# Optimization experiments

Measured on AMD Instinct MI355X. Metric: run time of the kernel, lower is better.

## Reference

```python
import jax, jax.numpy as jnp
import numpy as np

PATCH = [2, 4, 8, 16]   # square window sizes, one per head group
LAYERS = 2
C = 128                 # channel = d_input = hidden
DK = C // len(PATCH)    # 32 channels per head group


def leaky(z):
    return jax.nn.leaky_relu(z, negative_slope=0.2)


def conv2d(x, w, b, dil=1, pad=1):
    # x: (N,C,H,W), w: (O,I,3,3)
    y = jax.lax.conv_general_dilated(
        x, w, window_strides=(1, 1), padding=((pad, pad), (pad, pad)),
        rhs_dilation=(dil, dil), dimension_numbers=('NCHW', 'OIHW', 'NCHW'))
    return y + b[None, :, None, None]


def window_attn(q, k, v, bsz, ph, pw):
    # q/k/v: (b*t, dk, h, w) -> attention over t*oh*ow patch tokens of dim dk*ph*pw
    bt, dk, h, w = q.shape
    t = bt // bsz
    oh, ow = h // ph, w // pw

    def to_tok(z):
        z = z.reshape(bsz, t, dk, oh, ph, ow, pw)
        z = z.transpose(0, 1, 3, 5, 2, 4, 6)  # (b, t, oh, ow, dk, ph, pw)
        return z.reshape(bsz, t * oh * ow, dk * ph * pw)

    qt, kt, vt = to_tok(q), to_tok(k), to_tok(v)
    scale = 1.0 / jnp.sqrt(jnp.asarray(qt.shape[-1], qt.dtype))
    scores = jnp.einsum('bld,bmd->blm', qt, kt) * scale
    p = jax.nn.softmax(scores, axis=-1)
    y = jnp.einsum('blm,bmd->bld', p, vt)
    y = y.reshape(bsz, t, oh, ow, dk, ph, pw).transpose(0, 1, 4, 2, 5, 3, 6)
    return y.reshape(bt, dk, h, w)


def transformer_block(x, Wq, bq, Wk, bk, Wv, bv, Wo, bo, Wf1, bf1, Wf2, bf2, bsz):
    # 1x1 conv embeddings as channel matmuls
    q = jnp.einsum('bihw,oi->bohw', x, Wq) + bq[None, :, None, None]
    k = jnp.einsum('bihw,oi->bohw', x, Wk) + bk[None, :, None, None]
    v = jnp.einsum('bihw,oi->bohw', x, Wv) + bv[None, :, None, None]
    outs = []
    for g, p in enumerate(PATCH):
        sl = slice(g * DK, (g + 1) * DK)
        outs.append(window_attn(q[:, sl], k[:, sl], v[:, sl], bsz, p, p))
    att = jnp.concatenate(outs, axis=1)
    x = x + leaky(conv2d(att, Wo, bo, dil=1, pad=1))
    f = leaky(conv2d(x, Wf1, bf1, dil=2, pad=2))
    f = leaky(conv2d(f, Wf2, bf2, dil=1, pad=1))
    return x + f


def setup_inputs() -> dict:
    key = jax.random.key(0)
    ks = jax.random.split(key, 14)
    g = 0.02  # init gain matching init_weights normal(0, 0.02)
    x = jax.random.normal(ks[0], (8, C, 64, 64), dtype=jnp.float32)
    mk = lambda k, shape: (g * jax.random.normal(k, shape)).astype(jnp.float32)
    return {
        'x': x,
        'Wq': mk(ks[1], (LAYERS, C, C)), 'bq': jnp.zeros((LAYERS, C), jnp.float32),
        'Wk': mk(ks[2], (LAYERS, C, C)), 'bk': jnp.zeros((LAYERS, C), jnp.float32),
        'Wv': mk(ks[3], (LAYERS, C, C)), 'bv': jnp.zeros((LAYERS, C), jnp.float32),
        'Wo': mk(ks[4], (LAYERS, C, C, 3, 3)), 'bo': jnp.zeros((LAYERS, C), jnp.float32),
        'Wf1': mk(ks[5], (LAYERS, C, C, 3, 3)), 'bf1': jnp.zeros((LAYERS, C), jnp.float32),
        'Wf2': mk(ks[6], (LAYERS, C, C, 3, 3)), 'bf2': jnp.zeros((LAYERS, C), jnp.float32),
        'bsz': 2,
    }


def reference(x, Wq, bq, Wk, bk, Wv, bv, Wo, bo, Wf1, bf1, Wf2, bf2, bsz):
    for i in range(LAYERS):
        x = transformer_block(x, Wq[i], bq[i], Wk[i], bk[i], Wv[i], bv[i],
                              Wo[i], bo[i], Wf1[i], bf1[i], Wf2[i], bf2[i], bsz)
    return x
```

## Files before the change

kernel.cpp:

```cpp
#include <hip/hip_runtime.h>

__device__ __forceinline__ unsigned short f2bf(float f) {
  union { float f; unsigned int i; } c; c.f = f;
  unsigned int i = c.i;
  i += 0x7fffu + ((i >> 16) & 1u);
  return (unsigned short)(i >> 16);
}

typedef __attribute__((ext_vector_type(8))) short bf16x8;
typedef __attribute__((ext_vector_type(4))) float f32x4;


__global__ __launch_bounds__(256) void x2hwc(const float* __restrict__ X,
                                             unsigned short* __restrict__ Xh) {
  int pixg = blockIdx.x * 256 + threadIdx.x;
  int c0 = blockIdx.y * 8;
  int bt = pixg >> 12, pix = pixg & 4095;
  const float* src = X + ((size_t)bt << 19) + (size_t)c0 * 4096 + pix;
  unsigned int pk[4];
#pragma unroll
  for (int j = 0; j < 4; j++) {
    unsigned short u0 = f2bf(src[(2 * j) * 4096]);
    unsigned short u1 = f2bf(src[(2 * j + 1) * 4096]);
    pk[j] = (unsigned int)u0 | ((unsigned int)u1 << 16);
  }
  *(uint4*)(Xh + (size_t)pixg * 128 + c0) = make_uint4(pk[0], pk[1], pk[2], pk[3]);
}

__global__ __launch_bounds__(256) void wprep3(
    const float* __restrict__ s0, const float* __restrict__ s1,
    const float* __restrict__ s2, unsigned short* __restrict__ d0,
    unsigned short* __restrict__ d1, unsigned short* __restrict__ d2) {
  int idx = blockIdx.x * 256 + threadIdx.x;
  const float* s = blockIdx.y == 0 ? s0 : (blockIdx.y == 1 ? s1 : s2);
  unsigned short* d = blockIdx.y == 0 ? d0 : (blockIdx.y == 1 ? d1 : d2);
  int j = idx & 7;
  int lane = (idx >> 3) & 63;
  int kg = lane >> 4, ml = lane & 15;
  int f = idx >> 9;
  int mf = f & 3, wm = (f >> 2) & 1, cs = (f >> 3) & 3, tap = f >> 5;
  int o = wm * 64 + mf * 16 + ml;
  int i = cs * 32 + kg * 8 + j;
  d[idx] = f2bf(s[(size_t)(o * 128 + i) * 9 + tap]);
}

__global__ __launch_bounds__(256) void wprep1(
    const float* __restrict__ s0, const float* __restrict__ s1,
    const float* __restrict__ s2, unsigned short* __restrict__ d0,
    unsigned short* __restrict__ d1, unsigned short* __restrict__ d2) {
  int idx = blockIdx.x * 256 + threadIdx.x;
  const float* s = blockIdx.y == 0 ? s0 : (blockIdx.y == 1 ? s1 : s2);
  unsigned short* d = blockIdx.y == 0 ? d0 : (blockIdx.y == 1 ? d1 : d2);
  d[idx] = f2bf(s[idx]);
}

template <int MODE>
__global__ __launch_bounds__(256) void qkv_pack(
    const unsigned short* __restrict__ Xh, const unsigned short* __restrict__ Wb,
    const float* __restrict__ Bi, unsigned short* __restrict__ P,
    unsigned short* __restrict__ VtP, unsigned short* __restrict__ Ff) {
  int tid = threadIdx.x, lane = tid & 63, wid = tid >> 6;
  int wm = wid & 1, wn = wid >> 1;
  int ml = lane & 15, kg = lane >> 4;
  int m_base = blockIdx.y * 64 + wm * 32;
  int n_base = blockIdx.x * 64 + wn * 32;
  f32x4 acc[2][2];
#pragma unroll
  for (int i = 0; i < 2; i++)
#pragma unroll
    for (int j = 0; j < 2; j++) acc[i][j] = {0.f, 0.f, 0.f, 0.f};
#pragma unroll
  for (int kc = 0; kc < 128; kc += 32) {
    bf16x8 af[2], bfr[2];
#pragma unroll
    for (int mf = 0; mf < 2; mf++)
      af[mf] = *(const bf16x8*)(Wb + (size_t)(m_base + mf * 16 + ml) * 128 + kc + kg * 8);
#pragma unroll
    for (int nf = 0; nf < 2; nf++)
      bfr[nf] = *(const bf16x8*)(Xh + (size_t)(n_base + nf * 16 + ml) * 128 + kc + kg * 8);
#pragma unroll
    for (int mf = 0; mf < 2; mf++)
#pragma unroll
      for (int nf = 0; nf < 2; nf++)
        acc[mf][nf] = __builtin_amdgcn_mfma_f32_16x16x32_bf16(af[mf], bfr[nf], acc[mf][nf], 0, 0, 0);
  }
#pragma unroll
  for (int mf = 0; mf < 2; mf++)
#pragma unroll
    for (int nf = 0; nf < 2; nf++)
#pragma unroll
      for (int r = 0; r < 4; r++) {
        int c = m_base + mf * 16 + kg * 4 + r;
        int pixg = n_base + nf * 16 + ml;
        float val = acc[mf][nf][r] + Bi[c];
        int bt = pixg >> 12, pix = pixg & 4095;
        int h = pix >> 6, w = pix & 63;
        int g = c >> 5, sh = g + 1, msk = (1 << sh) - 1, ohn = 64 >> sh;
        int b = bt >> 2, t_i = bt & 3;
        int l = (t_i * ohn + (h >> sh)) * ohn + (w >> sh);
        int Dg = 32 << (2 * sh);
        int d = ((c & 31) << (2 * sh)) + ((h & msk) << sh) + (w & msk);
        if (MODE == 0) val *= rsqrtf((float)Dg);
        unsigned short bv = f2bf(val);
        size_t bofs = (size_t)b << 19;
        if (g == 0) {
          if (MODE == 0) {
            int qt = l >> 4, mlq = l & 15, cc = d >> 5, kgq = (d >> 3) & 3, j = d & 7;
            Ff[bofs + ((size_t)(qt * 4 + cc) << 9) + (kgq * 16 + mlq) * 8 + j] = bv;
          } else if (MODE == 1) {
            int ck = l >> 6, mfk = (l >> 4) & 3, mlk = l & 15;
            int cc = d >> 5, kgk = (d >> 3) & 3, j = d & 7;
            Ff[bofs + ((size_t)(ck * 16 + cc * 4 + mfk) << 9) + (kgk * 16 + mlk) * 8 + j] = bv;
          } else {
            int ck = l >> 6, part = (l >> 5) & 1, kgv = (l >> 3) & 3, j = l & 7;
            int nf = d >> 4, mlv = d & 15;
            Ff[bofs + ((size_t)(ck * 16 + nf * 2 + part) << 9) + (kgv * 16 + mlv) * 8 + j] = bv;
          }
        } else {
          size_t base = ((size_t)g << 20) + bofs;
          if (MODE != 2) {
            P[base + (size_t)l * Dg + d] = bv;
          } else {
            int Lg = 16384 >> (2 * sh);
            VtP[base + (size_t)d * Lg + l] = bv;
          }
        }
      }
}

__global__ __launch_bounds__(256) void gemm_tn(
    const unsigned short* __restrict__ A, const unsigned short* __restrict__ B,
    float* __restrict__ C, int K, int lda, int ldb, int ldc,
    long long sA, long long sB, long long sC) {
  int tid = threadIdx.x, lane = tid & 63, wid = tid >> 6;
  int wm = wid & 1, wn = wid >> 1;
  int ml = lane & 15, kg = lane >> 4;
  A += (size_t)blockIdx.z * sA;
  B += (size_t)blockIdx.z * sB;
  C += (size_t)blockIdx.z * sC;
  int m_base = blockIdx.y * 64 + wm * 32;
  int n_base = blockIdx.x * 64 + wn * 32;
  f32x4 acc[2][2];
#pragma unroll
  for (int i = 0; i < 2; i++)
#pragma unroll
    for (int j = 0; j < 2; j++) acc[i][j] = {0.f, 0.f, 0.f, 0.f};
  for (int kc = 0; kc < K; kc += 32) {
    bf16x8 af[2], bfr[2];
#pragma unroll
    for (int mf = 0; mf < 2; mf++)
      af[mf] = *(const bf16x8*)(A + (size_t)(m_base + mf * 16 + ml) * lda + kc + kg * 8);
#pragma unroll
    for (int nf = 0; nf < 2; nf++)
      bfr[nf] = *(const bf16x8*)(B + (size_t)(n_base + nf * 16 + ml) * ldb + kc + kg * 8);
#pragma unroll
    for (int mf = 0; mf < 2; mf++)
#pragma unroll
      for (int nf = 0; nf < 2; nf++)
        acc[mf][nf] = __builtin_amdgcn_mfma_f32_16x16x32_bf16(af[mf], bfr[nf], acc[mf][nf], 0, 0, 0);
  }
#pragma unroll
  for (int mf = 0; mf < 2; mf++)
#pragma unroll
    for (int nf = 0; nf < 2; nf++)
#pragma unroll
      for (int r = 0; r < 4; r++) {
        int m = m_base + mf * 16 + kg * 4 + r;
        int n = n_base + nf * 16 + ml;
        C[(size_t)m * ldc + n] = acc[mf][nf][r];
      }
}

__global__ __launch_bounds__(256) void gemm_tn_sk(
    const unsigned short* __restrict__ A, const unsigned short* __restrict__ B,
    float* __restrict__ Cp, int lda, int ldb, int L,
    long long sA, long long sB) {
  constexpr int KC = 128;
  int tid = threadIdx.x, lane = tid & 63, wid = tid >> 6;
  int wm = wid & 1, wn = wid >> 1;
  int ml = lane & 15, kg = lane >> 4;
  int bz = blockIdx.z, b = bz & 1, split = bz >> 1;
  A += (size_t)b * sA + split * KC;
  B += (size_t)b * sB + split * KC;
  float* Ct = Cp + (size_t)bz * L * L;
  int m_base = blockIdx.y * 64 + wm * 32;
  int n_base = blockIdx.x * 64 + wn * 32;
  f32x4 acc[2][2];
#pragma unroll
  for (int i = 0; i < 2; i++)
#pragma unroll
    for (int j = 0; j < 2; j++) acc[i][j] = {0.f, 0.f, 0.f, 0.f};
#pragma unroll
  for (int kc = 0; kc < KC; kc += 32) {
    bf16x8 af[2], bfr[2];
#pragma unroll
    for (int mf = 0; mf < 2; mf++)
      af[mf] = *(const bf16x8*)(A + (size_t)(m_base + mf * 16 + ml) * lda + kc + kg * 8);
#pragma unroll
    for (int nf = 0; nf < 2; nf++)
      bfr[nf] = *(const bf16x8*)(B + (size_t)(n_base + nf * 16 + ml) * ldb + kc + kg * 8);
#pragma unroll
    for (int mf = 0; mf < 2; mf++)
#pragma unroll
      for (int nf = 0; nf < 2; nf++)
        acc[mf][nf] = __builtin_amdgcn_mfma_f32_16x16x32_bf16(af[mf], bfr[nf], acc[mf][nf], 0, 0, 0);
  }
#pragma unroll
  for (int mf = 0; mf < 2; mf++)
#pragma unroll
    for (int nf = 0; nf < 2; nf++)
#pragma unroll
      for (int r = 0; r < 4; r++) {
        int m = m_base + mf * 16 + kg * 4 + r;
        int n = n_base + nf * 16 + ml;
        Ct[(size_t)m * L + n] = acc[mf][nf][r];
      }
}

__global__ __launch_bounds__(256) void gemm_tn_sk2(
    const unsigned short* __restrict__ A, const unsigned short* __restrict__ B,
    float* __restrict__ Cp, int KC, int lda, int ldb, int ldc,
    long long sA, long long sB) {
  int tid = threadIdx.x, lane = tid & 63, wid = tid >> 6;
  int wm = wid & 1, wn = wid >> 1;
  int ml = lane & 15, kg = lane >> 4;
  int bz = blockIdx.z, b = bz & 1, split = bz >> 1;
  A += (size_t)b * sA + (size_t)split * KC;
  B += (size_t)b * sB + (size_t)split * KC;
  size_t MN = (size_t)gridDim.y * 64 * ldc;
  float* Ct = Cp + (size_t)bz * MN;
  int m_base = blockIdx.y * 64 + wm * 32;
  int n_base = blockIdx.x * 64 + wn * 32;
  f32x4 acc[2][2];
#pragma unroll
  for (int i = 0; i < 2; i++)
#pragma unroll
    for (int j = 0; j < 2; j++) acc[i][j] = {0.f, 0.f, 0.f, 0.f};
  for (int kc = 0; kc < KC; kc += 32) {
    bf16x8 af[2], bfr[2];
#pragma unroll
    for (int mf = 0; mf < 2; mf++)
      af[mf] = *(const bf16x8*)(A + (size_t)(m_base + mf * 16 + ml) * lda + kc + kg * 8);
#pragma unroll
    for (int nf = 0; nf < 2; nf++)
      bfr[nf] = *(const bf16x8*)(B + (size_t)(n_base + nf * 16 + ml) * ldb + kc + kg * 8);
#pragma unroll
    for (int mf = 0; mf < 2; mf++)
#pragma unroll
      for (int nf = 0; nf < 2; nf++)
        acc[mf][nf] = __builtin_amdgcn_mfma_f32_16x16x32_bf16(af[mf], bfr[nf], acc[mf][nf], 0, 0, 0);
  }
#pragma unroll
  for (int mf = 0; mf < 2; mf++)
#pragma unroll
    for (int nf = 0; nf < 2; nf++)
#pragma unroll
      for (int r = 0; r < 4; r++) {
        int m = m_base + mf * 16 + kg * 4 + r;
        int n = n_base + nf * 16 + ml;
        Ct[(size_t)m * ldc + n] = acc[mf][nf][r];
      }
}

__global__ __launch_bounds__(256) void sum2(const float* __restrict__ Cp,
                                            float* __restrict__ Out,
                                            int MNq, long long sOut) {
  int idx = blockIdx.x * 256 + threadIdx.x;
  int b = idx / MNq, r = idx - b * MNq;
  const float4* c4 = (const float4*)Cp;
  float4 v0 = c4[(size_t)b * MNq + r];
  float4 v1 = c4[(size_t)(2 + b) * MNq + r];
  float4 o = make_float4(v0.x + v1.x, v0.y + v1.y, v0.z + v1.z, v0.w + v1.w);
  ((float4*)(Out + (size_t)b * sOut))[r] = o;
}

__global__ __launch_bounds__(256) void softmax_sum_bf16(
    const float* __restrict__ Sp, unsigned short* __restrict__ P, int L, int nsplit) {
  __shared__ float red[256];
  int tid = threadIdx.x;
  int b = blockIdx.x / L, m = blockIdx.x - b * L;
  const float* row = Sp + ((size_t)b * L + m) * L;
  long long pstride = 2LL * L * L;
  float val = 0.f;
  if (tid < L) {
    for (int s = 0; s < nsplit; s++) val += row[(size_t)s * pstride + tid];
  }
  red[tid] = (tid < L) ? val : -1e30f;
  __syncthreads();
  for (int s = 128; s > 0; s >>= 1) {
    if (tid < s) red[tid] = fmaxf(red[tid], red[tid + s]);
    __syncthreads();
  }
  float mx = red[0]; __syncthreads();
  float e = (tid < L) ? __expf(val - mx) : 0.f;
  red[tid] = e; __syncthreads();
  for (int s = 128; s > 0; s >>= 1) {
    if (tid < s) red[tid] += red[tid + s];
    __syncthreads();
  }
  float inv = 1.f / red[0];
  if (tid < L) P[((size_t)b * L + m) * L + tid] = f2bf(e * inv);
}

__global__ __launch_bounds__(256) void softmax_bf16(float* __restrict__ S,
                                                    unsigned short* __restrict__ P, int L) {
  __shared__ float red[256];
  int tid = threadIdx.x;
  float* p = S + (size_t)blockIdx.x * L;
  unsigned short* o = P + (size_t)blockIdx.x * L;
  float mx = -1e30f;
  for (int e = tid; e < L; e += 256) mx = fmaxf(mx, p[e]);
  red[tid] = mx; __syncthreads();
  for (int s = 128; s > 0; s >>= 1) {
    if (tid < s) red[tid] = fmaxf(red[tid], red[tid + s]);
    __syncthreads();
  }
  mx = red[0]; __syncthreads();
  float sm = 0.f;
  for (int e = tid; e < L; e += 256) {
    float v = __expf(p[e] - mx);
    p[e] = v; sm += v;
  }
  red[tid] = sm; __syncthreads();
  for (int s = 128; s > 0; s >>= 1) {
    if (tid < s) red[tid] += red[tid + s];
    __syncthreads();
  }
  float inv = 1.f / red[0];
  for (int e = tid; e < L; e += 256) o[e] = f2bf(p[e] * inv);
}

__global__ __launch_bounds__(256, 3) void flash_mfma(
    const unsigned short* __restrict__ Qf, const unsigned short* __restrict__ Kf,
    const unsigned short* __restrict__ Vf, float* __restrict__ Opart,
    float* __restrict__ MLp) {
  __shared__ float Ot[4][16][128];
  __shared__ unsigned short Pl[4][16][72];
  __shared__ float Ml[4][16], Ll[4][16];
  int tid = threadIdx.x, lane = tid & 63, wv = tid >> 6;
  int ml = lane & 15, kg = lane >> 4;
  int b = blockIdx.x >> 8, qt = blockIdx.x & 255;
  int half = blockIdx.y;
  size_t bofs = (size_t)b << 19;
  int q0 = qt * 16;

  bf16x8 qf[4];
#pragma unroll
  for (int cc = 0; cc < 4; cc++)
    qf[cc] = *(const bf16x8*)(Qf + bofs + ((size_t)(qt * 4 + cc) << 9) + lane * 8);

  float m_i = -1e30f, l_i = 0.f;
  f32x4 of[8];
#pragma unroll
  for (int nf = 0; nf < 8; nf++) of[nf] = {0.f, 0.f, 0.f, 0.f};

  int ck0 = half * 32 + wv * 8;
  for (int ck = ck0; ck < ck0 + 8; ck++) {
    const unsigned short* Kc = Kf + bofs + ((size_t)ck << 13);
    const unsigned short* Vc = Vf + bofs + ((size_t)ck << 13);
    f32x4 st[4];
#pragma unroll
    for (int mf = 0; mf < 4; mf++) st[mf] = {0.f, 0.f, 0.f, 0.f};
    __builtin_amdgcn_s_setprio(1);
#pragma unroll
    for (int cc = 0; cc < 4; cc++)
#pragma unroll
      for (int mf = 0; mf < 4; mf++) {
        bf16x8 kf = *(const bf16x8*)(Kc + ((cc * 4 + mf) << 9) + lane * 8);
        st[mf] = __builtin_amdgcn_mfma_f32_16x16x32_bf16(kf, qf[cc], st[mf], 0, 0, 0);
      }
    __builtin_amdgcn_s_setprio(0);
    bf16x8 vf[16];
#pragma unroll
    for (int nv = 0; nv < 16; nv++)
      vf[nv] = *(const bf16x8*)(Vc + (nv << 9) + lane * 8);
    float cmax = -1e30f;
#pragma unroll
    for (int mf = 0; mf < 4; mf++)
#pragma unroll
      for (int r = 0; r < 4; r++) cmax = fmaxf(cmax, st[mf][r]);
    cmax = fmaxf(cmax, __shfl_xor(cmax, 16));
    cmax = fmaxf(cmax, __shfl_xor(cmax, 32));
    int skip = __all(cmax <= m_i);
    float mnew = skip ? m_i : fmaxf(m_i, cmax);
    float p[4][4];
    float psum = 0.f;
#pragma unroll
    for (int mf = 0; mf < 4; mf++)
#pragma unroll
      for (int r = 0; r < 4; r++) {
        float pv = __expf(st[mf][r] - mnew);
        p[mf][r] = pv; psum += pv;
      }
    psum += __shfl_xor(psum, 16);
    psum += __shfl_xor(psum, 32);
    if (skip) {
      l_i += psum;
    } else {
      float alpha = __expf(m_i - mnew);
      l_i = l_i * alpha + psum;
      m_i = mnew;
      float a0 = __shfl(alpha, kg * 4 + 0), a1 = __shfl(alpha, kg * 4 + 1);
      float a2 = __shfl(alpha, kg * 4 + 2), a3 = __shfl(alpha, kg * 4 + 3);
#pragma unroll
      for (int nf = 0; nf < 8; nf++) {
        of[nf][0] *= a0; of[nf][1] *= a1; of[nf][2] *= a2; of[nf][3] *= a3;
      }
    }
#pragma unroll
    for (int mf = 0; mf < 4; mf++) {
      unsigned int lo = (unsigned int)f2bf(p[mf][0]) | ((unsigned int)f2bf(p[mf][1]) << 16);
      unsigned int hi = (unsigned int)f2bf(p[mf][2]) | ((unsigned int)f2bf(p[mf][3]) << 16);
      *(uint2*)&Pl[wv][ml][mf * 16 + kg * 4] = make_uint2(lo, hi);
    }
    bf16x8 pa0 = *(const bf16x8*)&Pl[wv][ml][kg * 8];
    bf16x8 pa1 = *(const bf16x8*)&Pl[wv][ml][32 + kg * 8];
    __builtin_amdgcn_s_setprio(1);
#pragma unroll
    for (int nf = 0; nf < 8; nf++) {
      of[nf] = __builtin_amdgcn_mfma_f32_16x16x32_bf16(pa0, vf[nf * 2 + 0], of[nf], 0, 0, 0);
      of[nf] = __builtin_amdgcn_mfma_f32_16x16x32_bf16(pa1, vf[nf * 2 + 1], of[nf], 0, 0, 0);
    }
    __builtin_amdgcn_s_setprio(0);
  }

  if (kg == 0) { Ml[wv][ml] = m_i; Ll[wv][ml] = l_i; }
  __syncthreads();
  float m0 = Ml[0][ml], m1 = Ml[1][ml], m2 = Ml[2][ml], m3 = Ml[3][ml];
  float mt = fmaxf(fmaxf(m0, m1), fmaxf(m2, m3));
  float lt = Ll[0][ml] * __expf(m0 - mt) + Ll[1][ml] * __expf(m1 - mt) +
             Ll[2][ml] * __expf(m2 - mt) + Ll[3][ml] * __expf(m3 - mt);
  float s = __expf(m_i - mt);
  float s0 = __shfl(s, kg * 4 + 0), s1 = __shfl(s, kg * 4 + 1);
  float s2 = __shfl(s, kg * 4 + 2), s3 = __shfl(s, kg * 4 + 3);
#pragma unroll
  for (int nf = 0; nf < 8; nf++) {
    Ot[wv][kg * 4 + 0][nf * 16 + ml] = of[nf][0] * s0;
    Ot[wv][kg * 4 + 1][nf * 16 + ml] = of[nf][1] * s1;
    Ot[wv][kg * 4 + 2][nf * 16 + ml] = of[nf][2] * s2;
    Ot[wv][kg * 4 + 3][nf * 16 + ml] = of[nf][3] * s3;
  }
  if (wv == 0 && kg == 0) {
    MLp[half * 16384 + b * 8192 + q0 + ml] = mt;
    MLp[half * 16384 + b * 8192 + 4096 + q0 + ml] = lt;
  }
  __syncthreads();
  int base = tid * 8;
  int q = base >> 7, d = base & 127;
  float4 r0 = make_float4(0, 0, 0, 0), r1 = make_float4(0, 0, 0, 0);
#pragma unroll
  for (int w = 0; w < 4; w++) {
    float4 a = *(const float4*)&Ot[w][q][d];
    float4 c = *(const float4*)&Ot[w][q][d + 4];
    r0.x += a.x; r0.y += a.y; r0.z += a.z; r0.w += a.w;
    r1.x += c.x; r1.y += c.y; r1.z += c.z; r1.w += c.w;
  }
  float* Op = Opart + ((size_t)half << 20) + bofs + (size_t)(q0 + q) * 128 + d;
  *(float4*)Op = r0;
  *(float4*)(Op + 4) = r1;
}

__global__ __launch_bounds__(256) void flash_merge(
    const float* __restrict__ Op, const float* __restrict__ MLp,
    float* __restrict__ O) {
  int idx = blockIdx.x * 256 + threadIdx.x;
  int b = idx >> 17, rem = idx & 131071;
  int q = rem >> 5, d4 = (rem & 31) << 2;
  float M0 = MLp[b * 8192 + q], L0 = MLp[b * 8192 + 4096 + q];
  float M1 = MLp[16384 + b * 8192 + q], L1 = MLp[16384 + b * 8192 + 4096 + q];
  float M = fmaxf(M0, M1);
  float e0 = __expf(M0 - M), e1 = __expf(M1 - M);
  float inv = 1.f / (e0 * L0 + e1 * L1);
  size_t o0 = ((size_t)b << 19) + (size_t)q * 128 + d4;
  float4 a = *(const float4*)(Op + o0);
  float4 c = *(const float4*)(Op + (1 << 20) + o0);
  float4 r = make_float4((e0 * a.x + e1 * c.x) * inv, (e0 * a.y + e1 * c.y) * inv,
                         (e0 * a.z + e1 * c.z) * inv, (e0 * a.w + e1 * c.w) * inv);
  *(float4*)(O + o0) = r;
}

__global__ __launch_bounds__(256) void unpack_att_bf16(
    const float* __restrict__ opk, unsigned short* __restrict__ att) {
  int idx = blockIdx.x * 256 + threadIdx.x;
  int oct = idx & 15, pix = idx >> 4;
  int w = pix & 63, h = (pix >> 6) & 63, bt = pix >> 12;
  int c0 = oct * 8;
  int g = c0 >> 5;
  int sh = g + 1, msk = (1 << sh) - 1;
  int ohn = 64 >> sh;
  int b = bt >> 2, t_i = bt & 3;
  int l = (t_i * ohn + (h >> sh)) * ohn + (w >> sh);
  int Dg = 32 << (2 * sh);
  int dbase = ((c0 & 31) << (2 * sh)) + ((h & msk) << sh) + (w & msk);
  const float* src = opk + ((size_t)g << 20) + ((size_t)b << 19) + (size_t)l * Dg;
  int dstep = 1 << (2 * sh);
  unsigned int pk[4];
#pragma unroll
  for (int j = 0; j < 4; j++) {
    unsigned short u0 = f2bf(src[dbase + (2 * j) * dstep]);
    unsigned short u1 = f2bf(src[dbase + (2 * j + 1) * dstep]);
    pk[j] = (unsigned int)u0 | ((unsigned int)u1 << 16);
  }
  *(uint4*)(att + ((size_t)pix * 128 + c0)) = make_uint4(pk[0], pk[1], pk[2], pk[3]);
}

template <int DIL, bool WF32, bool WBF16, bool RES>
__global__ __launch_bounds__(256) void conv_mfma(
    const unsigned short* __restrict__ Xb,
    const unsigned short* __restrict__ Wt,
    const float* __restrict__ Bi,
    const float* __restrict__ Rs,
    float* __restrict__ Yf,
    unsigned short* __restrict__ Ybf) {
  __shared__ __align__(16) char Xs[3 * 17408];
  int tid = threadIdx.x;
  int lane = tid & 63, wid = tid >> 6;
  int wm = wid & 1, wn = wid >> 1;
  int ml = lane & 15, kg = lane >> 4;
  int bt = blockIdx.x >> 6, h = blockIdx.x & 63;
  const int wbase = wn * 32;

  for (int idx = tid; idx < 3264; idx += 256) {
    int row = idx / 1088, rem = idx - row * 1088;
    int pix = rem >> 4, cs = rem & 15;
    int r = h + (row - 1) * DIL;
    int w = pix - 2;
    bf16x8 v = {0, 0, 0, 0, 0, 0, 0, 0};
    if ((unsigned)r < 64u && (unsigned)w < 64u)
      v = *(const bf16x8*)(Xb + (((size_t)(bt * 64 + r) * 64 + w) << 7) + cs * 8);
    int sw = (cs & 8) | ((cs ^ (pix & 7)) & 7);
    *(bf16x8*)(&Xs[row * 17408 + pix * 256 + sw * 16]) = v;
  }
  __syncthreads();

  f32x4 acc[4][2];
#pragma unroll
  for (int i = 0; i < 4; i++)
#pragma unroll
    for (int j = 0; j < 2; j++)
      acc[i][j] = {0.f, 0.f, 0.f, 0.f};

#pragma unroll
  for (int kh = 0; kh < 3; kh++) {
#pragma unroll
    for (int kw = 0; kw < 3; kw++) {
      int shf = (kw - 1) * DIL + 2;
#pragma unroll
      for (int cs4 = 0; cs4 < 4; cs4++) {
        const unsigned short* Ap =
            Wt + ((size_t)(((kh * 3 + kw) * 4 + cs4) * 2 + wm) << 11) + lane * 8;
        bf16x8 a[4], bfr[2];
#pragma unroll
        for (int mf = 0; mf < 4; mf++)
          a[mf] = *(const bf16x8*)(Ap + (mf << 9));
#pragma unroll
        for (int nf = 0; nf < 2; nf++) {
          int px = wbase + nf * 16 + ml + shf;
          int cslot = cs4 * 4 + kg;
          int sw = (cslot & 8) | ((cslot ^ (px & 7)) & 7);
          bfr[nf] = *(const bf16x8*)(&Xs[kh * 17408 + px * 256 + sw * 16]);
        }
#pragma unroll
        for (int mf = 0; mf < 4; mf++)
#pragma unroll
          for (int nf = 0; nf < 2; nf++)
            acc[mf][nf] = __builtin_amdgcn_mfma_f32_16x16x32_bf16(
                a[mf], bfr[nf], acc[mf][nf], 0, 0, 0);
      }
    }
  }

#pragma unroll
  for (int mf = 0; mf < 4; mf++) {
    int obase = wm * 64 + mf * 16 + kg * 4;
#pragma unroll
    for (int nf = 0; nf < 2; nf++) {
      int w = wbase + nf * 16 + ml;
      float v[4];
#pragma unroll
      for (int r4 = 0; r4 < 4; r4++) {
        int o = obase + r4;
        float val = acc[mf][nf][r4] + Bi[o];
        val = val > 0.f ? val : 0.2f * val;
        size_t idx = (((size_t)bt * 128 + o) * 64 + h) * 64 + w;
        if (RES) val += Rs[idx];
        if (WF32) Yf[idx] = val;
        v[r4] = val;
      }
      if (WBF16) {
        unsigned int lo = (unsigned int)f2bf(v[0]) | ((unsigned int)f2bf(v[1]) << 16);
        unsigned int hi = (unsigned int)f2bf(v[2]) | ((unsigned int)f2bf(v[3]) << 16);
        *(uint2*)(Ybf + (((size_t)bt * 4096 + h * 64 + w) * 128 + obase)) =
            make_uint2(lo, hi);
      }
    }
  }
}

extern "C" void kernel_launch(void* const* d_in, const int* in_sizes, int n_in,
                              void* d_out, int out_size, void* d_ws, size_t ws_size,
                              hipStream_t stream) {
  (void)in_sizes; (void)n_in; (void)out_size; (void)ws_size;
  const float* x   = (const float*)d_in[0];
  const float* Wq  = (const float*)d_in[1];
  const float* bq  = (const float*)d_in[2];
  const float* Wk  = (const float*)d_in[3];
  const float* bk  = (const float*)d_in[4];
  const float* Wv  = (const float*)d_in[5];
  const float* bv  = (const float*)d_in[6];
  const float* Wo  = (const float*)d_in[7];
  const float* bo  = (const float*)d_in[8];
  const float* Wf1 = (const float*)d_in[9];
  const float* bf1 = (const float*)d_in[10];
  const float* Wf2 = (const float*)d_in[11];
  const float* bf2 = (const float*)d_in[12];
  float* out = (float*)d_out;

  char* wsb = (char*)d_ws;
  float* xcur = (float*)(wsb);
  float* opk  = (float*)(wsb + 16777216);
  float* S    = (float*)(wsb + 33554432);
  unsigned short* Qp = (unsigned short*)(wsb + 41943040);
  unsigned short* Kp = (unsigned short*)(wsb + 50331648);
  unsigned short* Vt = (unsigned short*)(wsb + 58720256);
  unsigned short* Qf = (unsigned short*)(wsb + 67108864);
  unsigned short* Kf = (unsigned short*)(wsb + 69206016);
  unsigned short* Vf = (unsigned short*)(wsb + 71303168);
  unsigned short* att_hwc  = (unsigned short*)(wsb + 73400320);
  unsigned short* xcur_hwc = (unsigned short*)(wsb + 81788928);
  unsigned short* Wt0 = (unsigned short*)(wsb + 90177536);
  unsigned short* Wt1 = (unsigned short*)(wsb + 90472448);
  unsigned short* Wt2 = (unsigned short*)(wsb + 90767360);
  unsigned short* Wqb = (unsigned short*)(wsb + 91062272);
  unsigned short* Wkb = (unsigned short*)(wsb + 91095040);
  unsigned short* Wvb = (unsigned short*)(wsb + 91127808);
  float* MLp = (float*)(wsb + 91160576);
  unsigned short* f1_hwc = att_hwc;
  unsigned short* Pb = xcur_hwc;

  hipMemcpyAsync(xcur, x, 16777216, hipMemcpyDeviceToDevice, stream);

  const int Ls[3] = {1024, 256, 64};
  const int Ds[3] = {512, 2048, 8192};
  dim3 blk(256);

  x2hwc<<<dim3(128, 16), blk, 0, stream>>>(x, xcur_hwc);

  for (int layer = 0; layer < 2; layer++) {
    const float* wq  = Wq  + layer * 16384;
    const float* wk  = Wk  + layer * 16384;
    const float* wv  = Wv  + layer * 16384;
    const float* bq_ = bq  + layer * 128;
    const float* bk_ = bk  + layer * 128;
    const float* bv_ = bv  + layer * 128;
    const float* wo  = Wo  + layer * 147456;
    const float* bo_ = bo  + layer * 128;
    const float* wf1 = Wf1 + layer * 147456;
    const float* bf1_ = bf1 + layer * 128;
    const float* wf2 = Wf2 + layer * 147456;
    const float* bf2_ = bf2 + layer * 128;

    wprep3<<<dim3(576, 3), blk, 0, stream>>>(wo, wf1, wf2, Wt0, Wt1, Wt2);
    wprep1<<<dim3(64, 3), blk, 0, stream>>>(wq, wk, wv, Wqb, Wkb, Wvb);

    qkv_pack<0><<<dim3(512, 2), blk, 0, stream>>>(xcur_hwc, Wqb, bq_, Qp, nullptr, Qf);
    qkv_pack<1><<<dim3(512, 2), blk, 0, stream>>>(xcur_hwc, Wkb, bk_, Kp, nullptr, Kf);
    qkv_pack<2><<<dim3(512, 2), blk, 0, stream>>>(xcur_hwc, Wvb, bv_, nullptr, Vt, Vf);

    flash_mfma<<<dim3(512, 2), blk, 0, stream>>>(Qf, Kf, Vf, S, MLp);
    flash_merge<<<dim3(1024), blk, 0, stream>>>(S, MLp, opk);

    for (int gg = 0; gg < 3; gg++) {
      int g = gg + 1;
      size_t go = (size_t)g << 20;
      int L = Ls[gg], D = Ds[gg];
      if (gg == 0) {
        gemm_tn<<<dim3(L / 64, L / 64, 2), blk, 0, stream>>>(
            Qp + go, Kp + go, S, D, D, D, L, 1LL << 19, 1LL << 19, (long long)L * L);
        softmax_bf16<<<dim3(2 * L), blk, 0, stream>>>(S, Pb, L);
      } else {
        int nsplit = D / 128;
        gemm_tn_sk<<<dim3(L / 64, L / 64, 2 * nsplit), blk, 0, stream>>>(
            Qp + go, Kp + go, S, D, D, L, 1LL << 19, 1LL << 19);
        softmax_sum_bf16<<<dim3(2 * L), blk, 0, stream>>>(S, Pb, L, nsplit);
      }
      if (gg == 2) {
        gemm_tn<<<dim3(D / 64, L / 64, 2), blk, 0, stream>>>(
            Pb, Vt + go, opk + go, L, L, L, D, (long long)L * L, 1LL << 19, 1LL << 19);
      } else {
        gemm_tn_sk2<<<dim3(D / 64, L / 64, 4), blk, 0, stream>>>(
            Pb, Vt + go, S, L / 2, L, L, D, (long long)L * L, 1LL << 19);
        sum2<<<dim3(1024), blk, 0, stream>>>(S, opk + go, 131072, 1LL << 19);
      }
    }

    unpack_att_bf16<<<dim3(2048), blk, 0, stream>>>(opk, att_hwc);

    conv_mfma<1, true, true, true><<<dim3(512), blk, 0, stream>>>(
        att_hwc, Wt0, bo_, xcur, xcur, xcur_hwc);
    conv_mfma<2, false, true, false><<<dim3(512), blk, 0, stream>>>(
        xcur_hwc, Wt1, bf1_, nullptr, nullptr, f1_hwc);
    if (layer == 0) {
      conv_mfma<1, true, true, true><<<dim3(512), blk, 0, stream>>>(
          f1_hwc, Wt2, bf2_, xcur, xcur, xcur_hwc);
    } else {
      conv_mfma<1, true, false, true><<<dim3(512), blk, 0, stream>>>(
          f1_hwc, Wt2, bf2_, xcur, out, nullptr);
    }
  }
}
```

Before: 665.3 us.

## Split flash attention keys into four grid quarters with one query tile per wave

The flash kernel now gives each wave its own 16-query tile. The four waves in a block walk the same key chunks, and keys are split four ways across the grid. This replaces the old scheme, where the four waves of a block split keys for a single query tile and then reduced through LDS. Dropping that LDS reduction and the extra barriers is meant to help, and waves sharing K/V chunks should reuse them in cache. The cost is four partial outputs written to global memory (one reuses the att_hwc buffer as scratch), a wider 4-way merge kernel, a per-iteration __syncthreads, and lower occupancy from launch_bounds 2.

After: 664.1 us. No clear change (-0.2%).

```diff
diff --git a/kernel.cpp b/kernel.cpp
--- a/kernel.cpp
+++ b/kernel.cpp
@@ -330,17 +330,16 @@
   for (int e = tid; e < L; e += 256) o[e] = f2bf(p[e] * inv);
 }
 
-__global__ __launch_bounds__(256, 3) void flash_mfma(
+__global__ __launch_bounds__(256, 2) void flash_mfma(
     const unsigned short* __restrict__ Qf, const unsigned short* __restrict__ Kf,
-    const unsigned short* __restrict__ Vf, float* __restrict__ Opart,
-    float* __restrict__ MLp) {
-  __shared__ float Ot[4][16][128];
+    const unsigned short* __restrict__ Vf, float* __restrict__ O01,
+    float* __restrict__ O23, float* __restrict__ MLp) {
   __shared__ unsigned short Pl[4][16][72];
-  __shared__ float Ml[4][16], Ll[4][16];
   int tid = threadIdx.x, lane = tid & 63, wv = tid >> 6;
   int ml = lane & 15, kg = lane >> 4;
-  int b = blockIdx.x >> 8, qt = blockIdx.x & 255;
-  int half = blockIdx.y;
+  int b = blockIdx.x >> 6, qt4 = blockIdx.x & 63;
+  int qt = qt4 * 4 + wv;
+  int quarter = blockIdx.y;
   size_t bofs = (size_t)b << 19;
   int q0 = qt * 16;
 
@@ -354,8 +353,8 @@
 #pragma unroll
   for (int nf = 0; nf < 8; nf++) of[nf] = {0.f, 0.f, 0.f, 0.f};
 
-  int ck0 = half * 32 + wv * 8;
-  for (int ck = ck0; ck < ck0 + 8; ck++) {
+  for (int ck = quarter * 16; ck < quarter * 16 + 16; ck++) {
+    __syncthreads();
     const unsigned short* Kc = Kf + bofs + ((size_t)ck << 13);
     const unsigned short* Vc = Vf + bofs + ((size_t)ck << 13);
     f32x4 st[4];
@@ -424,58 +423,51 @@
     __builtin_amdgcn_s_setprio(0);
   }
 
-  if (kg == 0) { Ml[wv][ml] = m_i; Ll[wv][ml] = l_i; }
-  __syncthreads();
-  float m0 = Ml[0][ml], m1 = Ml[1][ml], m2 = Ml[2][ml], m3 = Ml[3][ml];
-  float mt = fmaxf(fmaxf(m0, m1), fmaxf(m2, m3));
-  float lt = Ll[0][ml] * __expf(m0 - mt) + Ll[1][ml] * __expf(m1 - mt) +
-             Ll[2][ml] * __expf(m2 - mt) + Ll[3][ml] * __expf(m3 - mt);
-  float s = __expf(m_i - mt);
-  float s0 = __shfl(s, kg * 4 + 0), s1 = __shfl(s, kg * 4 + 1);
-  float s2 = __shfl(s, kg * 4 + 2), s3 = __shfl(s, kg * 4 + 3);
-#pragma unroll
-  for (int nf = 0; nf < 8; nf++) {
-    Ot[wv][kg * 4 + 0][nf * 16 + ml] = of[nf][0] * s0;
-    Ot[wv][kg * 4 + 1][nf * 16 + ml] = of[nf][1] * s1;
-    Ot[wv][kg * 4 + 2][nf * 16 + ml] = of[nf][2] * s2;
-    Ot[wv][kg * 4 + 3][nf * 16 + ml] = of[nf][3] * s3;
-  }
-  if (wv == 0 && kg == 0) {
-    MLp[half * 16384 + b * 8192 + q0 + ml] = mt;
-    MLp[half * 16384 + b * 8192 + 4096 + q0 + ml] = lt;
-  }
-  __syncthreads();
-  int base = tid * 8;
-  int q = base >> 7, d = base & 127;
-  float4 r0 = make_float4(0, 0, 0, 0), r1 = make_float4(0, 0, 0, 0);
-#pragma unroll
-  for (int w = 0; w < 4; w++) {
-    float4 a = *(const float4*)&Ot[w][q][d];
-    float4 c = *(const float4*)&Ot[w][q][d + 4];
-    r0.x += a.x; r0.y += a.y; r0.z += a.z; r0.w += a.w;
-    r1.x += c.x; r1.y += c.y; r1.z += c.z; r1.w += c.w;
-  }
-  float* Op = Opart + ((size_t)half << 20) + bofs + (size_t)(q0 + q) * 128 + d;
-  *(float4*)Op = r0;
-  *(float4*)(Op + 4) = r1;
-}
-
-__global__ __launch_bounds__(256) void flash_merge(
-    const float* __restrict__ Op, const float* __restrict__ MLp,
-    float* __restrict__ O) {
+  float* Op = (quarter < 2) ? (O01 + ((size_t)quarter << 20))
+                            : (O23 + ((size_t)(quarter - 2) << 20));
+  if (kg == 0) {
+    MLp[quarter * 16384 + b * 8192 + q0 + ml] = m_i;
+    MLp[quarter * 16384 + b * 8192 + 4096 + q0 + ml] = l_i;
+  }
+#pragma unroll
+  for (int nf = 0; nf < 8; nf++)
+#pragma unroll
+    for (int r = 0; r < 4; r++)
+      Op[bofs + (size_t)(q0 + kg * 4 + r) * 128 + nf * 16 + ml] = of[nf][r];
+}
+
+__global__ __launch_bounds__(256) void flash_merge4(
+    const float* __restrict__ O01, const float* __restrict__ O23,
+    const float* __restrict__ MLp, float* __restrict__ O) {
   int idx = blockIdx.x * 256 + threadIdx.x;
   int b = idx >> 17, rem = idx & 131071;
   int q = rem >> 5, d4 = (rem & 31) << 2;
-  float M0 = MLp[b * 8192 + q], L0 = MLp[b * 8192 + 4096 + q];
-  float M1 = MLp[16384 + b * 8192 + q], L1 = MLp[16384 + b * 8192 + 4096 + q];
-  float M = fmaxf(M0, M1);
-  float e0 = __expf(M0 - M), e1 = __expf(M1 - M);
-  float inv = 1.f / (e0 * L0 + e1 * L1);
+  float Ms[4], Ls[4];
+  float M = -1e30f;
+#pragma unroll
+  for (int s = 0; s < 4; s++) {
+    Ms[s] = MLp[s * 16384 + b * 8192 + q];
+    Ls[s] = MLp[s * 16384 + b * 8192 + 4096 + q];
+    M = fmaxf(M, Ms[s]);
+  }
+  float es[4];
+  float den = 0.f;
+#pragma unroll
+  for (int s = 0; s < 4; s++) {
+    es[s] = __expf(Ms[s] - M);
+    den += es[s] * Ls[s];
+  }
+  float inv = 1.f / den;
   size_t o0 = ((size_t)b << 19) + (size_t)q * 128 + d4;
-  float4 a = *(const float4*)(Op + o0);
-  float4 c = *(const float4*)(Op + (1 << 20) + o0);
-  float4 r = make_float4((e0 * a.x + e1 * c.x) * inv, (e0 * a.y + e1 * c.y) * inv,
-                         (e0 * a.z + e1 * c.z) * inv, (e0 * a.w + e1 * c.w) * inv);
+  float4 a0 = *(const float4*)(O01 + o0);
+  float4 a1 = *(const float4*)(O01 + (1 << 20) + o0);
+  float4 a2 = *(const float4*)(O23 + o0);
+  float4 a3 = *(const float4*)(O23 + (1 << 20) + o0);
+  float4 r;
+  r.x = (es[0] * a0.x + es[1] * a1.x + es[2] * a2.x + es[3] * a3.x) * inv;
+  r.y = (es[0] * a0.y + es[1] * a1.y + es[2] * a2.y + es[3] * a3.y) * inv;
+  r.z = (es[0] * a0.z + es[1] * a1.z + es[2] * a2.z + es[3] * a3.z) * inv;
+  r.w = (es[0] * a0.w + es[1] * a1.w + es[2] * a2.w + es[3] * a3.w) * inv;
   *(float4*)(O + o0) = r;
 }
 
@@ -637,6 +629,7 @@
   float* MLp = (float*)(wsb + 91160576);
   unsigned short* f1_hwc = att_hwc;
   unsigned short* Pb = xcur_hwc;
+  float* Opart23 = (float*)att_hwc;
 
   hipMemcpyAsync(xcur, x, 16777216, hipMemcpyDeviceToDevice, stream);
 
@@ -667,8 +660,8 @@
     qkv_pack<1><<<dim3(512, 2), blk, 0, stream>>>(xcur_hwc, Wkb, bk_, Kp, nullptr, Kf);
     qkv_pack<2><<<dim3(512, 2), blk, 0, stream>>>(xcur_hwc, Wvb, bv_, nullptr, Vt, Vf);
 
-    flash_mfma<<<dim3(512, 2), blk, 0, stream>>>(Qf, Kf, Vf, S, MLp);
-    flash_merge<<<dim3(1024), blk, 0, stream>>>(S, MLp, opk);
+    flash_mfma<<<dim3(128, 4), blk, 0, stream>>>(Qf, Kf, Vf, S, Opart23, MLp);
+    flash_merge4<<<dim3(1024), blk, 0, stream>>>(S, Opart23, MLp, opk);
 
     for (int gg = 0; gg < 3; gg++) {
       int g = gg + 1;
```
